# Optimization experiments

Measured on AMD Instinct MI355X. Metric: run time of the kernel, lower is better.

Reference implementation:

```python
import jax, jax.numpy as jnp
import numpy as np

B, T, I, H, O = 256, 512, 512, 512, 1


def setup_inputs() -> dict:
    key = jax.random.key(0)
    ks = jax.random.split(key, 9)
    xavier = lambda k, shape: jax.random.uniform(
        k, shape, jnp.float32,
        -jnp.sqrt(6.0 / (shape[0] + shape[1])), jnp.sqrt(6.0 / (shape[0] + shape[1])))
    return {
        "x":   jax.random.normal(ks[0], (B, T, I), jnp.float32),
        "Wg":  xavier(ks[1], (I + H, 2 * H)),
        "bg":  jnp.zeros((2 * H,), jnp.float32),
        "Wh":  xavier(ks[2], (I + H, H)),
        "bh":  jnp.zeros((H,), jnp.float32),
        "Wo1": xavier(ks[3], (H, H // 2)),
        "bo1": jnp.zeros((H // 2,), jnp.float32),
        "Wo2": xavier(ks[4], (H // 2, O)),
        "bo2": jnp.zeros((O,), jnp.float32),
    }


def reference(x, Wg, bg, Wh, bh, Wo1, bo1, Wo2, bo2):
    # x: [B, T, I]; GRU-style recurrence with fused gate matmul per step.
    Bsz = x.shape[0]
    Hd = Wh.shape[1]

    def step(h, xt):
        xh = jnp.concatenate([xt, h], axis=-1)              # [B, I+H]
        gates = xh @ Wg + bg                                 # [B, 2H]
        update = jax.nn.sigmoid(gates[:, :Hd])
        reset = jax.nn.sigmoid(gates[:, Hd:])
        cand = jnp.tanh(jnp.concatenate([xt, reset * h], axis=-1) @ Wh + bh)
        h_new = (1.0 - update) * h + update * cand
        y = jax.nn.relu(h_new @ Wo1 + bo1) @ Wo2 + bo2       # [B, O]
        return h_new, y

    h0 = jnp.zeros((Bsz, Hd), x.dtype)
    h_final, ys = jax.lax.scan(step, h0, jnp.swapaxes(x, 0, 1))  # ys: [T, B, O]
    return jnp.swapaxes(ys, 0, 1), h_final
```

## Files before the change

### kernel.cpp

```cpp
#include <hip/hip_runtime.h>
#include <hip/hip_bf16.h>
#include <stdint.h>

typedef float f32x4 __attribute__((ext_vector_type(4)));
typedef short bf16x8 __attribute__((ext_vector_type(8)));
typedef int   i32x4  __attribute__((ext_vector_type(4)));

#define DEVINL static __device__ __forceinline__

constexpr int BATCH = 256, SEQ = 512, IDIM = 512, HDIM = 512;
constexpr int NG = 8, WC = 32, RPG = 32, CPW = 16;

constexpr int WGS_OFF = 0;
constexpr int WHS_OFF = 65536;
constexpr int WO1_OFF = 98304;
constexpr int XPOSE_OFF = 114688;
constexpr int SMEM_BYTES = XPOSE_OFF + 2 * 640;

constexpr size_t WS_ZERO = 4096;
constexpr size_t HBF_OFF  = 8192;
constexpr size_t RHBF_OFF = HBF_OFF + 262144;
constexpr size_t WS_NEEDED = RHBF_OFF + 262144;

DEVINL short f2bf(float f) {
  uint32_t u = __float_as_uint(f);
  u += 0x7FFFu + ((u >> 16) & 1u);
  return (short)(u >> 16);
}
DEVINL int wgs_off(int c, int k) { return WGS_OFF + c * 2048 + ((k * 2) ^ ((c & 7) << 4)); }
DEVINL int whs_off(int c, int k) { return WHS_OFF + c * 2048 + ((k * 2) ^ ((c & 7) << 4)); }
DEVINL int wo1_off(int c, int k) { return WO1_OFF + c * 1024 + ((k * 2) ^ ((c & 7) << 4)); }
DEVINL float sigm(float v) { return 1.f / (1.f + __expf(-v)); }
DEVINL bf16x8 asbf(i32x4 v) { return __builtin_bit_cast(bf16x8, v); }

DEVINL void flag_pub(uint32_t* p, uint32_t v) {
  asm volatile("s_waitcnt vmcnt(0) lgkmcnt(0)\n\tglobal_store_dword %0, %1, off sc1"
               :: "v"(p), "v"(v) : "memory");
}
DEVINL void poll32(const uint32_t* base, uint32_t target) {
  const uint32_t* p = base + (threadIdx.x & 31);
  int iter = 0;
  for (;;) {
    uint32_t v;
    asm volatile("global_load_dword %0, %1, off sc1\n\ts_waitcnt vmcnt(0)"
                 : "=v"(v) : "v"(p) : "memory");
    if (__all((int)(v >= target))) break;
    if (++iter > 20000) break;
    __builtin_amdgcn_s_sleep(1);
  }
  __builtin_amdgcn_sched_barrier(0);
}
DEVINL void publish16x16(char* smem, int xpose, short* dst, int grow, int colbase,
                         int lane, const float* vals) {
  const int q = lane >> 4, lc = lane & 15;
#pragma unroll
  for (int ri = 0; ri < 4; ++ri)
    *(short*)(smem + xpose + (q * 4 + ri) * 40 + lc * 2) = f2bf(vals[ri]);
  asm volatile("s_waitcnt lgkmcnt(0)" ::: "memory");
  __builtin_amdgcn_sched_barrier(0);
  const int rl = lane >> 2, cq = lane & 3;
  unsigned long long d = *(const unsigned long long*)(smem + xpose + rl * 40 + cq * 8);
  short* gp = dst + (size_t)(grow + rl) * HDIM + colbase + cq * 4;
  asm volatile("global_store_dwordx2 %0, %1, off sc1" :: "v"(gp), "v"(d) : "memory");
}
#define GLD16(dst, ptr, imm) \
  asm volatile("global_load_dwordx4 %0, %1, off offset:" imm " sc1" : "=v"(dst) : "v"(ptr))
#define GLD_ALL16(arr, ptr) do { \
  GLD16(arr[0],  ptr, "0");   GLD16(arr[1],  ptr, "64");  \
  GLD16(arr[2],  ptr, "128"); GLD16(arr[3],  ptr, "192"); \
  GLD16(arr[4],  ptr, "256"); GLD16(arr[5],  ptr, "320"); \
  GLD16(arr[6],  ptr, "384"); GLD16(arr[7],  ptr, "448"); \
  GLD16(arr[8],  ptr, "512"); GLD16(arr[9],  ptr, "576"); \
  GLD16(arr[10], ptr, "640"); GLD16(arr[11], ptr, "704"); \
  GLD16(arr[12], ptr, "768"); GLD16(arr[13], ptr, "832"); \
  GLD16(arr[14], ptr, "896"); GLD16(arr[15], ptr, "960"); \
  asm volatile("s_waitcnt vmcnt(0)" ::: "memory"); \
  __builtin_amdgcn_sched_barrier(0); \
} while (0)

#define MFMA(a, b, c) __builtin_amdgcn_mfma_f32_16x16x32_bf16((a), (b), (c), 0, 0, 0)
#define LDB(off) (*(const bf16x8*)(smem + (off)))

__global__ void __launch_bounds__(256, 1) init_ys_kernel(float* out, const float* bo2) {
  int i = blockIdx.x * 256 + threadIdx.x;
  if (i < BATCH * SEQ) out[i] = bo2[0];
}

__global__ void __launch_bounds__(128, 1) gru_persist(
    const float* __restrict__ x,  const float* __restrict__ Wg, const float* __restrict__ bg,
    const float* __restrict__ Wh, const float* __restrict__ bh,
    const float* __restrict__ Wo1,const float* __restrict__ bo1,
    const float* __restrict__ Wo2,const float* __restrict__ bo2,
    float* __restrict__ out, char* __restrict__ ws)
{
  extern __shared__ char smem[];
  const int bid  = blockIdx.x;
  const int gi   = bid & 7;
  const int j    = bid >> 3;
  const int tid  = threadIdx.x;
  const int lane = tid & 63;
  const int mt   = tid >> 6;
  const int rowbase = gi * RPG;
  const int colbase = j * CPW;

  short* hbf  = (short*)(ws + HBF_OFF);
  short* rhbf = (short*)(ws + RHBF_OFF);
  uint32_t* fA = (uint32_t*)(ws + (size_t)gi * 512);
  uint32_t* fB = (uint32_t*)(ws + (size_t)gi * 512 + 256);
  const uint32_t* fAmine = fA + mt * 32;
  const uint32_t* fBmine = fB + mt * 32;
  uint32_t* myA = fA + (mt * 32 + j);
  uint32_t* myB = fB + (mt * 32 + j);

  for (int it = 0; it < 256; ++it) {
    int cc = tid & 31;
    int k = (tid >> 5) + it * 4;
    int cg = (cc < 16) ? (colbase + cc) : (512 + colbase + (cc - 16));
    *(short*)(smem + wgs_off(cc, k)) = f2bf(Wg[(size_t)k * 1024 + cg]);
  }
  for (int it = 0; it < 128; ++it) {
    int cc = tid & 15;
    int k = (tid >> 4) + it * 8;
    *(short*)(smem + whs_off(cc, k)) = f2bf(Wh[(size_t)k * 512 + colbase + cc]);
  }
  for (int it = 0; it < 64; ++it) {
    int cc = tid & 15;
    int k = (tid >> 4) + it * 8;
    *(short*)(smem + wo1_off(cc, k)) = (cc < 8) ? f2bf(Wo1[(size_t)k * 256 + j * 8 + cc]) : (short)0;
  }

  const int lc = lane & 15;
  const float bgu  = bg[colbase + lc];
  const float bgr  = bg[512 + colbase + lc];
  const float bhc  = bh[colbase + lc];
  const float bo1c = (lc < 8) ? bo1[j * 8 + lc] : 0.f;
  const float wo2c = (lc < 8) ? Wo2[j * 8 + lc] : 0.f;
  __syncthreads();

  const int arow  = mt * 16 + lc;
  const int kl    = (lane >> 4) * 8;
  const int xpose = XPOSE_OFF + mt * 640;
  const int grow  = rowbase + mt * 16;

  const char* hfrag  = (const char*)(hbf  + (size_t)(rowbase + arow) * HDIM + kl);
  const char* rhfrag = (const char*)(rhbf + (size_t)(rowbase + arow) * HDIM + kl);

  float hreg[4] = {0.f, 0.f, 0.f, 0.f};
  for (int t = 0; t < SEQ; ++t) {
    bf16x8 xa[16];
    {
      const float* xrow = x + ((size_t)(rowbase + arow) * SEQ + t) * IDIM + kl;
#pragma unroll
      for (int ks = 0; ks < 16; ++ks) {
        float4 a = *(const float4*)(xrow + ks * 32);
        float4 b = *(const float4*)(xrow + ks * 32 + 4);
        bf16x8 v;
        v[0] = f2bf(a.x); v[1] = f2bf(a.y); v[2] = f2bf(a.z); v[3] = f2bf(a.w);
        v[4] = f2bf(b.x); v[5] = f2bf(b.y); v[6] = f2bf(b.z); v[7] = f2bf(b.w);
        xa[ks] = v;
      }
    }
    f32x4 gu0 = {0,0,0,0}, gu1 = {0,0,0,0}, gr0 = {0,0,0,0}, gr1 = {0,0,0,0};
#pragma unroll
    for (int ks = 0; ks < 16; ks += 2) {
      gu0 = MFMA(xa[ks],   LDB(wgs_off(lc, ks * 32 + kl)),            gu0);
      gu1 = MFMA(xa[ks+1], LDB(wgs_off(lc, (ks + 1) * 32 + kl)),      gu1);
      gr0 = MFMA(xa[ks],   LDB(wgs_off(16 + lc, ks * 32 + kl)),       gr0);
      gr1 = MFMA(xa[ks+1], LDB(wgs_off(16 + lc, (ks + 1) * 32 + kl)), gr1);
    }
    i32x4 ha[16];
    if (t) {
      poll32(fBmine, (uint32_t)t);
      GLD_ALL16(ha, hfrag);
#pragma unroll
      for (int ks = 0; ks < 16; ks += 2) {
        gu0 = MFMA(asbf(ha[ks]),   LDB(wgs_off(lc, 512 + ks * 32 + kl)),            gu0);
        gu1 = MFMA(asbf(ha[ks+1]), LDB(wgs_off(lc, 512 + (ks + 1) * 32 + kl)),      gu1);
        gr0 = MFMA(asbf(ha[ks]),   LDB(wgs_off(16 + lc, 512 + ks * 32 + kl)),       gr0);
        gr1 = MFMA(asbf(ha[ks+1]), LDB(wgs_off(16 + lc, 512 + (ks + 1) * 32 + kl)), gr1);
      }
    }
    f32x4 gu = gu0 + gu1, gr = gr0 + gr1;
    float uv[4], rhv[4];
#pragma unroll
    for (int ri = 0; ri < 4; ++ri) {
      uv[ri]  = sigm(gu[ri] + bgu);
      rhv[ri] = sigm(gr[ri] + bgr) * hreg[ri];
    }
    if (t) {
      publish16x16(smem, xpose, rhbf, grow, colbase, lane, rhv);
      flag_pub(myA, (uint32_t)(t + 1));
    }
    f32x4 hd0 = {0,0,0,0}, hd1 = {0,0,0,0};
    if (t) {
#pragma unroll
      for (int ks = 0; ks < 16; ks += 2) {
        hd0 = MFMA(asbf(ha[ks]),   LDB(wo1_off(lc, ks * 32 + kl)),       hd0);
        hd1 = MFMA(asbf(ha[ks+1]), LDB(wo1_off(lc, (ks + 1) * 32 + kl)), hd1);
      }
    }
    f32x4 cx0 = {0,0,0,0}, cx1 = {0,0,0,0};
#pragma unroll
    for (int ks = 0; ks < 16; ks += 2) {
      cx0 = MFMA(xa[ks],   LDB(whs_off(lc, ks * 32 + kl)),       cx0);
      cx1 = MFMA(xa[ks+1], LDB(whs_off(lc, (ks + 1) * 32 + kl)), cx1);
    }
    f32x4 ch0 = {0,0,0,0}, ch1 = {0,0,0,0};
    if (t) {
      poll32(fAmine, (uint32_t)(t + 1));
      i32x4 ra[16];
      GLD_ALL16(ra, rhfrag);
#pragma unroll
      for (int ks = 0; ks < 16; ks += 2) {
        ch0 = MFMA(asbf(ra[ks]),   LDB(whs_off(lc, 512 + ks * 32 + kl)),       ch0);
        ch1 = MFMA(asbf(ra[ks+1]), LDB(whs_off(lc, 512 + (ks + 1) * 32 + kl)), ch1);
      }
    }
    f32x4 cc = cx0 + cx1 + ch0 + ch1;
    float hnv[4];
#pragma unroll
    for (int ri = 0; ri < 4; ++ri) {
      float cand = tanhf(cc[ri] + bhc);
      float hnew = hreg[ri] + uv[ri] * (cand - hreg[ri]);
      hreg[ri] = hnew; hnv[ri] = hnew;
      if (t == SEQ - 1) {
        int row = mt * 16 + (lane >> 4) * 4 + ri;
        out[(size_t)(BATCH * SEQ) + (size_t)(rowbase + row) * HDIM + colbase + lc] = hnew;
      }
    }
    publish16x16(smem, xpose, hbf, grow, colbase, lane, hnv);
    flag_pub(myB, (uint32_t)(t + 1));
    if (t) {
      f32x4 d = hd0 + hd1;
#pragma unroll
      for (int ri = 0; ri < 4; ++ri) {
        float z = fmaxf(d[ri] + bo1c, 0.f) * wo2c;
        z += __shfl_xor(z, 1); z += __shfl_xor(z, 2);
        z += __shfl_xor(z, 4); z += __shfl_xor(z, 8);
        if (lc == 0) {
          int row = rowbase + mt * 16 + (lane >> 4) * 4 + ri;
          unsafeAtomicAdd(&out[(size_t)row * SEQ + (t - 1)], z);
        }
      }
    }
  }
  poll32(fBmine, (uint32_t)SEQ);
  i32x4 ha[16];
  GLD_ALL16(ha, hfrag);
  f32x4 hd0 = {0,0,0,0}, hd1 = {0,0,0,0};
#pragma unroll
  for (int ks = 0; ks < 16; ks += 2) {
    hd0 = MFMA(asbf(ha[ks]),   LDB(wo1_off(lc, ks * 32 + kl)),       hd0);
    hd1 = MFMA(asbf(ha[ks+1]), LDB(wo1_off(lc, (ks + 1) * 32 + kl)), hd1);
  }
  f32x4 d = hd0 + hd1;
#pragma unroll
  for (int ri = 0; ri < 4; ++ri) {
    float z = fmaxf(d[ri] + bo1c, 0.f) * wo2c;
    z += __shfl_xor(z, 1); z += __shfl_xor(z, 2);
    z += __shfl_xor(z, 4); z += __shfl_xor(z, 8);
    if (lc == 0) {
      int row = rowbase + mt * 16 + (lane >> 4) * 4 + ri;
      unsafeAtomicAdd(&out[(size_t)row * SEQ + (SEQ - 1)], z);
    }
  }
}

extern "C" void kernel_launch(void* const* d_in, const int* in_sizes, int n_in,
                              void* d_out, int out_size, void* d_ws, size_t ws_size,
                              hipStream_t stream) {
  const float* x   = (const float*)d_in[0];
  const float* Wg  = (const float*)d_in[1];
  const float* bg  = (const float*)d_in[2];
  const float* Wh  = (const float*)d_in[3];
  const float* bh  = (const float*)d_in[4];
  const float* Wo1 = (const float*)d_in[5];
  const float* bo1 = (const float*)d_in[6];
  const float* Wo2 = (const float*)d_in[7];
  const float* bo2 = (const float*)d_in[8];
  float* out = (float*)d_out;
  char*  ws  = (char*)d_ws;
  if (ws_size < WS_NEEDED) return;

  hipMemsetAsync(ws, 0, WS_ZERO, stream);
  init_ys_kernel<<<dim3(512), dim3(256), 0, stream>>>(out, bo2);

  (void)hipFuncSetAttribute((const void*)gru_persist,
                            hipFuncAttributeMaxDynamicSharedMemorySize, SMEM_BYTES);

  gru_persist<<<dim3(NG * WC), dim3(128), SMEM_BYTES, stream>>>(
      x, Wg, bg, Wh, bh, Wo1, bo1, Wo2, bo2, out, ws);
}
```

Baseline: 4.272 ms.

## Replace output atomics with per-column partial buffer plus finalize kernel; packed bf16 convert

Instead of float atomic adds into the output for each step's head projection, each of the 32 column workgroups writes its partial sum into a per-(row,t) slot of a workspace buffer. A separate finalize kernel sums the 32 partials and adds the bias. This applies only when the workspace is large enough, otherwise the atomic path is kept. The x load now converts to bf16 with a packed v_cvt_pk_bf16_f32 instead of manual rounding. The trade is 16 MB of extra workspace traffic and one extra launch in exchange for removing contended atomics from the recurrent loop.

```diff
diff --git a/kernel.cpp b/kernel.cpp
--- a/kernel.cpp
+++ b/kernel.cpp
@@ -5,6 +5,7 @@
 typedef float f32x4 __attribute__((ext_vector_type(4)));
 typedef short bf16x8 __attribute__((ext_vector_type(8)));
 typedef int   i32x4  __attribute__((ext_vector_type(4)));
+typedef unsigned int u32x4 __attribute__((ext_vector_type(4)));
 
 #define DEVINL static __device__ __forceinline__
 
@@ -17,15 +18,22 @@
 constexpr int XPOSE_OFF = 114688;
 constexpr int SMEM_BYTES = XPOSE_OFF + 2 * 640;
 
-constexpr size_t WS_ZERO = 4096;
+constexpr size_t WS_ZERO  = 4096;
 constexpr size_t HBF_OFF  = 8192;
 constexpr size_t RHBF_OFF = HBF_OFF + 262144;
-constexpr size_t WS_NEEDED = RHBF_OFF + 262144;
+constexpr size_t WS_ATOM  = RHBF_OFF + 262144;
+constexpr size_t YP_OFF   = WS_ATOM;
+constexpr size_t WS_PART  = YP_OFF + (size_t)BATCH * SEQ * 32 * 4;
 
 DEVINL short f2bf(float f) {
   uint32_t u = __float_as_uint(f);
   u += 0x7FFFu + ((u >> 16) & 1u);
   return (short)(u >> 16);
+}
+DEVINL uint32_t cvtpk(float lo, float hi) {
+  uint32_t r;
+  asm("v_cvt_pk_bf16_f32 %0, %1, %2" : "=v"(r) : "v"(lo), "v"(hi));
+  return r;
 }
 DEVINL int wgs_off(int c, int k) { return WGS_OFF + c * 2048 + ((k * 2) ^ ((c & 7) << 4)); }
 DEVINL int whs_off(int c, int k) { return WHS_OFF + c * 2048 + ((k * 2) ^ ((c & 7) << 4)); }
@@ -81,17 +89,40 @@
 #define MFMA(a, b, c) __builtin_amdgcn_mfma_f32_16x16x32_bf16((a), (b), (c), 0, 0, 0)
 #define LDB(off) (*(const bf16x8*)(smem + (off)))
 
+#define LOADCVT_X(tt) do { \
+  const float* xr_ = x + ((size_t)(rowbase + arow) * SEQ + (size_t)(tt)) * IDIM + kl; \
+  _Pragma("unroll") \
+  for (int ks = 0; ks < 16; ++ks) { \
+    float4 a_ = *(const float4*)(xr_ + ks * 32); \
+    float4 b_ = *(const float4*)(xr_ + ks * 32 + 4); \
+    u32x4 v_ = {cvtpk(a_.x, a_.y), cvtpk(a_.z, a_.w), \
+                cvtpk(b_.x, b_.y), cvtpk(b_.z, b_.w)}; \
+    xa[ks] = __builtin_bit_cast(bf16x8, v_); \
+  } \
+} while (0)
+
 __global__ void __launch_bounds__(256, 1) init_ys_kernel(float* out, const float* bo2) {
   int i = blockIdx.x * 256 + threadIdx.x;
   if (i < BATCH * SEQ) out[i] = bo2[0];
 }
 
+__global__ void __launch_bounds__(256, 1) finalize_ys_kernel(
+    const float* __restrict__ part, float* __restrict__ out, const float* __restrict__ bo2) {
+  int e = blockIdx.x * 256 + threadIdx.x;
+  const float4* p = (const float4*)(part + (size_t)e * 32);
+  float s = 0.f;
+#pragma unroll
+  for (int q = 0; q < 8; ++q) { float4 v = p[q]; s += v.x + v.y + v.z + v.w; }
+  out[e] = bo2[0] + s;
+}
+
+template<bool PART>
 __global__ void __launch_bounds__(128, 1) gru_persist(
     const float* __restrict__ x,  const float* __restrict__ Wg, const float* __restrict__ bg,
     const float* __restrict__ Wh, const float* __restrict__ bh,
     const float* __restrict__ Wo1,const float* __restrict__ bo1,
     const float* __restrict__ Wo2,const float* __restrict__ bo2,
-    float* __restrict__ out, char* __restrict__ ws)
+    float* __restrict__ out, char* __restrict__ ws, float* __restrict__ ypart)
 {
   extern __shared__ char smem[];
   const int bid  = blockIdx.x;
@@ -145,21 +176,10 @@
   const char* hfrag  = (const char*)(hbf  + (size_t)(rowbase + arow) * HDIM + kl);
   const char* rhfrag = (const char*)(rhbf + (size_t)(rowbase + arow) * HDIM + kl);
 
+  bf16x8 xa[16];
   float hreg[4] = {0.f, 0.f, 0.f, 0.f};
   for (int t = 0; t < SEQ; ++t) {
-    bf16x8 xa[16];
-    {
-      const float* xrow = x + ((size_t)(rowbase + arow) * SEQ + t) * IDIM + kl;
-#pragma unroll
-      for (int ks = 0; ks < 16; ++ks) {
-        float4 a = *(const float4*)(xrow + ks * 32);
-        float4 b = *(const float4*)(xrow + ks * 32 + 4);
-        bf16x8 v;
-        v[0] = f2bf(a.x); v[1] = f2bf(a.y); v[2] = f2bf(a.z); v[3] = f2bf(a.w);
-        v[4] = f2bf(b.x); v[5] = f2bf(b.y); v[6] = f2bf(b.z); v[7] = f2bf(b.w);
-        xa[ks] = v;
-      }
-    }
+    LOADCVT_X(t);
     f32x4 gu0 = {0,0,0,0}, gu1 = {0,0,0,0}, gr0 = {0,0,0,0}, gr1 = {0,0,0,0};
 #pragma unroll
     for (int ks = 0; ks < 16; ks += 2) {
@@ -239,7 +259,10 @@
         z += __shfl_xor(z, 4); z += __shfl_xor(z, 8);
         if (lc == 0) {
           int row = rowbase + mt * 16 + (lane >> 4) * 4 + ri;
-          unsafeAtomicAdd(&out[(size_t)row * SEQ + (t - 1)], z);
+          if constexpr (PART)
+            ypart[((size_t)row * SEQ + (t - 1)) * 32 + j] = z;
+          else
+            unsafeAtomicAdd(&out[(size_t)row * SEQ + (t - 1)], z);
         }
       }
     }
@@ -261,7 +284,10 @@
     z += __shfl_xor(z, 4); z += __shfl_xor(z, 8);
     if (lc == 0) {
       int row = rowbase + mt * 16 + (lane >> 4) * 4 + ri;
-      unsafeAtomicAdd(&out[(size_t)row * SEQ + (SEQ - 1)], z);
+      if constexpr (PART)
+        ypart[((size_t)row * SEQ + (SEQ - 1)) * 32 + j] = z;
+      else
+        unsafeAtomicAdd(&out[(size_t)row * SEQ + (SEQ - 1)], z);
     }
   }
 }
@@ -280,14 +306,25 @@
   const float* bo2 = (const float*)d_in[8];
   float* out = (float*)d_out;
   char*  ws  = (char*)d_ws;
-  if (ws_size < WS_NEEDED) return;
+  if (ws_size < WS_ATOM) return;
+
+  const bool part = (ws_size >= WS_PART);
+  float* ypart = (float*)(ws + YP_OFF);
 
   hipMemsetAsync(ws, 0, WS_ZERO, stream);
-  init_ys_kernel<<<dim3(512), dim3(256), 0, stream>>>(out, bo2);
-
-  (void)hipFuncSetAttribute((const void*)gru_persist,
-                            hipFuncAttributeMaxDynamicSharedMemorySize, SMEM_BYTES);
-
-  gru_persist<<<dim3(NG * WC), dim3(128), SMEM_BYTES, stream>>>(
-      x, Wg, bg, Wh, bh, Wo1, bo1, Wo2, bo2, out, ws);
-}
+  if (!part)
+    init_ys_kernel<<<dim3(512), dim3(256), 0, stream>>>(out, bo2);
+
+  if (part) {
+    (void)hipFuncSetAttribute((const void*)gru_persist<true>,
+                              hipFuncAttributeMaxDynamicSharedMemorySize, SMEM_BYTES);
+    gru_persist<true><<<dim3(NG * WC), dim3(128), SMEM_BYTES, stream>>>(
+        x, Wg, bg, Wh, bh, Wo1, bo1, Wo2, bo2, out, ws, ypart);
+    finalize_ys_kernel<<<dim3(512), dim3(256), 0, stream>>>(ypart, out, bo2);
+  } else {
+    (void)hipFuncSetAttribute((const void*)gru_persist<false>,
+                              hipFuncAttributeMaxDynamicSharedMemorySize, SMEM_BYTES);
+    gru_persist<false><<<dim3(NG * WC), dim3(128), SMEM_BYTES, stream>>>(
+        x, Wg, bg, Wh, bh, Wo1, bo1, Wo2, bo2, out, ws, ypart);
+  }
+}
```

Result: slower. 7.787 ms (+82.3%).
